# Optimization experiments

Hardware: AMD Instinct MI355X
Metric: run time of the kernel (lower is better)

## Reference

```python
import jax, jax.numpy as jnp
import numpy as np

N, E, G = 40000, 400000, 64
IN, ED, HID, HEADS, OUT = 2, 18, 64, 4, 3

def _glorot(key, shape):
    fan_in = shape[0]
    return jax.random.normal(key, shape, dtype=jnp.float32) / np.float32(np.sqrt(fan_in))

def setup_inputs():
    key = jax.random.key(0)
    ks = jax.random.split(key, 32)
    d1 = HEADS * HID  # 256
    return {
        "x": jax.random.normal(ks[0], (N, IN), jnp.float32),
        "edge_index": jax.random.randint(ks[1], (2, E), 0, N),
        "edge_attr": jax.random.normal(ks[2], (E, ED), jnp.float32),
        "batch": jnp.sort(jax.random.randint(ks[3], (N,), 0, G)),
        # conv1: TransformerConv(2 -> 64, heads=4, concat=True, beta=True, edge_dim=18)
        "Wq1": _glorot(ks[4], (IN, d1)), "bq1": jnp.zeros((d1,), jnp.float32),
        "Wk1": _glorot(ks[5], (IN, d1)), "bk1": jnp.zeros((d1,), jnp.float32),
        "Wv1": _glorot(ks[6], (IN, d1)), "bv1": jnp.zeros((d1,), jnp.float32),
        "We1": _glorot(ks[7], (ED, d1)),
        "Wskip1": _glorot(ks[8], (IN, d1)), "bskip1": jnp.zeros((d1,), jnp.float32),
        "Wbeta1": _glorot(ks[9], (3 * d1, 1)),
        # conv2: TransformerConv(256 -> 64, heads=1, concat=False, beta=True, edge_dim=18)
        "Wq2": _glorot(ks[10], (d1, HID)), "bq2": jnp.zeros((HID,), jnp.float32),
        "Wk2": _glorot(ks[11], (d1, HID)), "bk2": jnp.zeros((HID,), jnp.float32),
        "Wv2": _glorot(ks[12], (d1, HID)), "bv2": jnp.zeros((HID,), jnp.float32),
        "We2": _glorot(ks[13], (ED, HID)),
        "Wskip2": _glorot(ks[14], (d1, HID)), "bskip2": jnp.zeros((HID,), jnp.float32),
        "Wbeta2": _glorot(ks[15], (3 * HID, 1)),
        "Wlin": _glorot(ks[16], (HID, OUT)), "blin": jnp.zeros((OUT,), jnp.float32),
    }

def _tconv(x, src, dst, edge_attr, Wq, bq, Wk, bk, Wv, bv, We, Wskip, bskip, Wbeta, H, C, concat):
    # PyG TransformerConv with edge_dim, beta=True, root_weight=True (eval: dropout off)
    n = x.shape[0]
    q = (x @ Wq + bq).reshape(n, H, C)
    k = (x @ Wk + bk).reshape(n, H, C)
    v = (x @ Wv + bv).reshape(n, H, C)
    e = (edge_attr @ We).reshape(-1, H, C)              # [E,H,C]
    kj = k[src] + e                                      # key_j + edge
    alpha = jnp.einsum('ehc,ehc->eh', q[dst], kj) * (1.0 / (C ** 0.5))  # [E,H]
    # segment softmax over destination nodes
    amax = jax.ops.segment_max(alpha, dst, num_segments=n)
    ex = jnp.exp(alpha - amax[dst])
    den = jax.ops.segment_sum(ex, dst, num_segments=n)
    w = ex / (den[dst] + 1e-16)
    msg = (v[src] + e) * w[:, :, None]                   # [E,H,C]
    out = jax.ops.segment_sum(msg, dst, num_segments=n)  # [N,H,C]
    out = out.reshape(n, H * C) if concat else out.mean(axis=1)
    # beta-gated skip connection
    xr = x @ Wskip + bskip
    beta = jax.nn.sigmoid(jnp.concatenate([out, xr, out - xr], axis=-1) @ Wbeta)
    return beta * xr + (1.0 - beta) * out

def reference(x, edge_index, edge_attr, batch, Wq1, bq1, Wk1, bk1, Wv1, bv1, We1, Wskip1, bskip1, Wbeta1, Wq2, bq2, Wk2, bk2, Wv2, bv2, We2, Wskip2, bskip2, Wbeta2, Wlin, blin):
    src, dst = edge_index[0], edge_index[1]
    h = jax.nn.relu(_tconv(x, src, dst, edge_attr, Wq1, bq1, Wk1, bk1, Wv1, bv1, We1, Wskip1, bskip1, Wbeta1, HEADS, HID, True))
    h = jax.nn.relu(_tconv(h, src, dst, edge_attr, Wq2, bq2, Wk2, bk2, Wv2, bv2, We2, Wskip2, bskip2, Wbeta2, 1, HID, False))
    # global mean pool per graph
    s = jax.ops.segment_sum(h, batch, num_segments=G)
    cnt = jax.ops.segment_sum(jnp.ones((h.shape[0], 1), h.dtype), batch, num_segments=G)
    pooled = s / jnp.maximum(cnt, 1.0)
    return pooled @ Wlin + blin
```

## Files before the change

kernel.cpp:

```cpp
#include <hip/hip_runtime.h>
#include <hip/hip_fp16.h>

#define N_NODES 40000
#define N_EDGES 400000
#define N_GRAPHS 64
#define D1 256
#define HIDC 64
#define NHEADS 4
#define EDIM 18
#define EPAD 20
#define OUTF 3

typedef _Float16 f16x8 __attribute__((ext_vector_type(8)));
typedef float f32x4 __attribute__((ext_vector_type(4)));

__global__ void prep_w(const float* __restrict__ Wq, const float* __restrict__ bq,
                       const float* __restrict__ Wk, const float* __restrict__ bk,
                       const float* __restrict__ Wv, const float* __restrict__ bv,
                       const float* __restrict__ Ws, const float* __restrict__ bs,
                       const float* __restrict__ We2,
                       const float* __restrict__ Wq1, const float* __restrict__ bq1,
                       const float* __restrict__ Wk1, const float* __restrict__ bk1,
                       const float* __restrict__ We1,
                       __half* __restrict__ Bt, float* __restrict__ bias,
                       float* __restrict__ cbuf) {
    int c = blockIdx.x, k = threadIdx.x;
    if (c < 256) {
        int m = c >> 6, d = c & 63;
        const float* W = (m == 0) ? Wq : (m == 1) ? Wk : (m == 2) ? Wv : Ws;
        Bt[c * 256 + k] = __float2half(W[k * 64 + d]);
        if (k == 0) {
            const float* b = (m == 0) ? bq : (m == 1) ? bk : (m == 2) ? bv : bs;
            bias[c] = b[d];
        }
    } else if (c < 288) {
        int j = c - 256;
        float s = 0.f;
        if (j < EDIM)
            for (int cc = 0; cc < 64; ++cc) s += Wq[k * 64 + cc] * We2[j * 64 + cc];
        Bt[c * 256 + k] = __float2half(s);
        if (k == 0) {
            float b = 0.f;
            if (j < EDIM)
                for (int cc = 0; cc < 64; ++cc) b += bq[cc] * We2[j * 64 + cc];
            bias[c] = b;
        }
    } else {
        int t = k;
        if (t < 36) {
            int h = t / 9, r = t % 9, a = r / 3, b = r % 3;
            const float* A = (a == 0) ? Wq1 : (a == 1) ? Wq1 + D1 : bq1;
            const float* B = (b == 0) ? Wk1 : (b == 1) ? Wk1 + D1 : bk1;
            float s = 0.f;
            for (int cc = 0; cc < 64; ++cc) s += A[h * 64 + cc] * B[h * 64 + cc];
            cbuf[h * 63 + a * 3 + b] = s;
        } else if (t < 252) {
            int i = t - 36;
            int h = i / 54, rr = (i % 54) / 18, j = i % 18;
            const float* A = (rr == 0) ? Wq1 : (rr == 1) ? Wq1 + D1 : bq1;
            float s = 0.f;
            for (int cc = 0; cc < 64; ++cc) s += A[h * 64 + cc] * We1[j * D1 + h * 64 + cc];
            cbuf[h * 63 + 9 + rr * 18 + j] = s;
        }
    }
}

__global__ void initA(const float* __restrict__ x, const float* __restrict__ cbuf,
                      float* __restrict__ coef, float* __restrict__ acc1,
                      float* __restrict__ acc2, float* __restrict__ out2,
                      int* __restrict__ deg, float* __restrict__ pooled,
                      int* __restrict__ gs, int* __restrict__ ge) {
    int t = blockIdx.x * 256 + threadIdx.x;
    acc1[t] = 0.f;
    {
        int n = t / 84, r = t % 84, h = r / 21, c = r % 21;
        const float* cb = cbuf + h * 63;
        float x0 = x[2 * n], x1 = x[2 * n + 1], o;
        if (c < 3) o = x0 * cb[c] + x1 * cb[3 + c] + cb[6 + c];
        else { int j = c - 3; o = x0 * cb[9 + j] + x1 * cb[27 + j] + cb[45 + j]; }
        coef[t] = o;
    }
    if (t < N_NODES * 64) out2[t] = 0.f;
    if (t < N_NODES * 20) acc2[t] = 0.f;
    if (t < N_NODES) deg[t] = 0;
    if (t < N_GRAPHS * HIDC) pooled[t] = 0.f;
    if (t < N_GRAPHS) { gs[t] = 0; ge[t] = 0; }
}

__global__ void hist_kernel(const int* __restrict__ ei, int* __restrict__ deg) {
    int e = blockIdx.x * 256 + threadIdx.x;
    if (e < N_EDGES) atomicAdd(&deg[ei[N_EDGES + e]], 1);
}

__global__ void scanA(const int* __restrict__ deg, int* __restrict__ bsum) {
    __shared__ int s[256];
    int b = blockIdx.x, t = threadIdx.x;
    s[t] = (t < 160) ? deg[b * 160 + t] : 0;
    __syncthreads();
    for (int off = 128; off; off >>= 1) {
        if (t < off) s[t] += s[t + off];
        __syncthreads();
    }
    if (t == 0) bsum[b] = s[0];
}

__global__ void scanB(const int* __restrict__ bsum, int* __restrict__ boff) {
    __shared__ int s[256];
    int t = threadIdx.x;
    int v = (t < 250) ? bsum[t] : 0;
    s[t] = v;
    __syncthreads();
    for (int off = 1; off < 256; off <<= 1) {
        int add = (t >= off) ? s[t - off] : 0;
        __syncthreads();
        s[t] += add;
        __syncthreads();
    }
    if (t < 250) boff[t] = s[t] - v;
}

__global__ void scanC(const int* __restrict__ deg, const int* __restrict__ boff,
                      int* __restrict__ cursor) {
    __shared__ int s[256];
    int b = blockIdx.x, t = threadIdx.x;
    int v = (t < 160) ? deg[b * 160 + t] : 0;
    s[t] = v;
    __syncthreads();
    for (int off = 1; off < 256; off <<= 1) {
        int add = (t >= off) ? s[t - off] : 0;
        __syncthreads();
        s[t] += add;
        __syncthreads();
    }
    if (t < 160) cursor[b * 160 + t] = boff[b] + s[t] - v;
}

__global__ void perm_kernel(const int* __restrict__ ei, int* __restrict__ cursor,
                            int* __restrict__ inv) {
    int e = blockIdx.x * 256 + threadIdx.x;
    if (e >= N_EDGES) return;
    int p = atomicAdd(&cursor[ei[N_EDGES + e]], 1);
    inv[p] = e;
}

__global__ void gatherE(const int* __restrict__ inv, const int* __restrict__ ei,
                        const float* __restrict__ ea, const float* __restrict__ x,
                        const float* __restrict__ coef,
                        int* __restrict__ src_s, int* __restrict__ dst_s,
                        float* __restrict__ ea_s, float* __restrict__ alpha1) {
    int p = blockIdx.x * 256 + threadIdx.x;
    if (p >= N_EDGES) return;
    int e = inv[p];
    int src = ei[e], dst = ei[N_EDGES + e];
    src_s[p] = src;
    dst_s[p] = dst;
    const float* srow = ea + (size_t)e * EDIM;
    float s[EDIM];
    #pragma unroll
    for (int j = 0; j < EDIM; ++j) s[j] = srow[j];
    float x0 = x[src * 2], x1 = x[src * 2 + 1];
    float4* drow = (float4*)(ea_s + (size_t)p * EPAD);
    drow[0] = make_float4(s[0],  s[1],  s[2],  s[3]);
    drow[1] = make_float4(s[4],  s[5],  s[6],  s[7]);
    drow[2] = make_float4(s[8],  s[9],  s[10], s[11]);
    drow[3] = make_float4(s[12], s[13], s[14], s[15]);
    drow[4] = make_float4(s[16], s[17], x0, x1);
    const float* cb = coef + (size_t)dst * 84;
    #pragma unroll
    for (int h = 0; h < NHEADS; ++h) {
        const float* c = cb + h * 21;
        float a = x0 * c[0] + x1 * c[1] + c[2];
        #pragma unroll
        for (int j = 0; j < EDIM; ++j) a += s[j] * c[3 + j];
        alpha1[(size_t)h * N_EDGES + p] = __expf(a * 0.125f);
    }
}

__global__ void strip1(const int* __restrict__ dst_s, const float* __restrict__ alpha1,
                       const float* __restrict__ ea_s, float* __restrict__ acc1) {
    int t = threadIdx.x;
    int strip = blockIdx.x * 2 + (t >> 7);
    int gl = t & 127;
    bool active = gl < 84;
    int cgl = active ? gl : 83;
    int h = cgl / 21, comp = cgl % 21;
    int voff = (comp == 0) ? 18 : (comp == 1) ? 19 : (comp - 3);
    bool isone = (comp == 2);
    int p0 = strip * 16;
    int dsts[16]; float w[16]; float v[16];
    #pragma unroll
    for (int j = 0; j < 16; ++j) dsts[j] = dst_s[p0 + j];
    #pragma unroll
    for (int j = 0; j < 16; ++j) w[j] = alpha1[(size_t)h * N_EDGES + p0 + j];
    #pragma unroll
    for (int j = 0; j < 16; ++j) v[j] = isone ? 1.f : ea_s[(size_t)(p0 + j) * EPAD + voff];
    float acc = 0.f;
    int prev = dsts[0];
    #pragma unroll
    for (int j = 0; j < 16; ++j) {
        if (dsts[j] != prev) {
            if (active) atomicAdd(&acc1[(size_t)prev * 84 + gl], acc);
            acc = 0.f; prev = dsts[j];
        }
        acc += w[j] * v[j];
    }
    if (active) atomicAdd(&acc1[(size_t)prev * 84 + gl], acc);
}

__global__ void finalize1x(const float* __restrict__ x, const float* __restrict__ acc1,
                           const float* __restrict__ Wv, const float* __restrict__ bv,
                           const float* __restrict__ We, const float* __restrict__ Wskip,
                           const float* __restrict__ bskip, const float* __restrict__ Wbeta,
                           __half* __restrict__ h1f) {
    __shared__ float red[4][4];
    int nb = blockIdx.x * 4;
    int t = threadIdx.x;
    int h = t >> 6;
    float wv0 = Wv[t], wv1 = Wv[D1 + t], bvv = bv[t];
    float we[EDIM];
    #pragma unroll
    for (int j = 0; j < EDIM; ++j) we[j] = We[j * D1 + t];
    float ws0 = Wskip[t], ws1 = Wskip[D1 + t], bsv = bskip[t];
    float wb0 = Wbeta[t], wb1 = Wbeta[D1 + t], wb2 = Wbeta[2 * D1 + t];
    float o[4], xr[4], part[4];
    #pragma unroll
    for (int i = 0; i < 4; ++i) {
        int node = nb + i;
        const float* a = acc1 + (size_t)node * 84 + h * 21;
        float l = a[2];
        float oo = a[0] * wv0 + a[1] * wv1 + l * bvv;
        #pragma unroll
        for (int j = 0; j < EDIM; ++j) oo += a[3 + j] * we[j];
        oo /= (l + 1e-16f);
        float x0 = x[node * 2], x1 = x[node * 2 + 1];
        xr[i] = x0 * ws0 + x1 * ws1 + bsv;
        o[i] = oo;
        part[i] = oo * wb0 + xr[i] * wb1 + (oo - xr[i]) * wb2;
    }
    #pragma unroll
    for (int off = 32; off; off >>= 1) {
        #pragma unroll
        for (int i = 0; i < 4; ++i) part[i] += __shfl_xor(part[i], off);
    }
    if ((t & 63) == 0) {
        #pragma unroll
        for (int i = 0; i < 4; ++i) red[h][i] = part[i];
    }
    __syncthreads();
    #pragma unroll
    for (int i = 0; i < 4; ++i) {
        float tot = red[0][i] + red[1][i] + red[2][i] + red[3][i];
        float beta = 1.f / (1.f + __expf(-tot));
        h1f[(size_t)(nb + i) * D1 + t] =
            __float2half(fmaxf(beta * xr[i] + (1.f - beta) * o[i], 0.f));
    }
}

__device__ __forceinline__ void nl2_store(int c, int gr, float v,
        float* __restrict__ q2, float* __restrict__ k2, __half* __restrict__ v2h,
        float* __restrict__ xr2, float* __restrict__ qe) {
    if (c < 256) {
        int m = c >> 6, d = c & 63;
        if (m == 0)      q2[(size_t)gr * 64 + d] = v;
        else if (m == 1) k2[(size_t)gr * 64 + d] = v;
        else if (m == 2) v2h[(size_t)gr * 64 + d] = __float2half(v);
        else             xr2[(size_t)gr * 64 + d] = v;
    } else {
        qe[(size_t)gr * 32 + (c - 256)] = v;
    }
}

__global__ __launch_bounds__(256) void nl2_mfma(
        const __half* __restrict__ h1f, const __half* __restrict__ Bt,
        const float* __restrict__ bias,
        float* __restrict__ q2, float* __restrict__ k2,
        __half* __restrict__ v2h, float* __restrict__ xr2,
        float* __restrict__ qe) {
    int W = blockIdx.x * 4 + (threadIdx.x >> 6);
    if (W >= 18 * 313) return;
    int ct = W % 18, chunk = W / 18;
    int lane = threadIdx.x & 63, quad = lane >> 4, mm = lane & 15;
    int c0 = ct * 16 + mm;
    const _Float16* Ap = (const _Float16*)h1f;
    const _Float16* Bp = (const _Float16*)Bt;
    const _Float16* b0 = Bp + (size_t)c0 * 256 + quad * 8;
    f16x8 b[8];
    #pragma unroll
    for (int s = 0; s < 8; ++s) b[s] = *(const f16x8*)(b0 + s * 32);
    float bz = bias[c0];
    int rt_end = chunk * 8 + 8; if (rt_end > 2500) rt_end = 2500;
    for (int rt = chunk * 8; rt < rt_end; ++rt) {
        int row0 = rt * 16;
        const _Float16* arow = Ap + (size_t)(row0 + mm) * 256 + quad * 8;
        f16x8 a[8];
        #pragma unroll
        for (int s = 0; s < 8; ++s) a[s] = *(const f16x8*)(arow + s * 32);
        f32x4 accA = {bz, bz, bz, bz};
        f32x4 accB = {0.f, 0.f, 0.f, 0.f};
        #pragma unroll
        for (int s = 0; s < 4; ++s) {
            accA = __builtin_amdgcn_mfma_f32_16x16x32_f16(a[s],     b[s],     accA, 0, 0, 0);
            accB = __builtin_amdgcn_mfma_f32_16x16x32_f16(a[s + 4], b[s + 4], accB, 0, 0, 0);
        }
        #pragma unroll
        for (int r = 0; r < 4; ++r) {
            int gr = row0 + quad * 4 + r;
            nl2_store(c0, gr, accA[r] + accB[r], q2, k2, v2h, xr2, qe);
        }
    }
}

#define LG2_BLOCKS 2048
#define LG2_WAVES (LG2_BLOCKS * 4)
__global__ void logits2(const int* __restrict__ src_s, const int* __restrict__ dst_s,
                        const float* __restrict__ ea_s, const float* __restrict__ q2,
                        const float* __restrict__ k2, const float* __restrict__ qe,
                        float* __restrict__ alpha2) {
    int t = threadIdx.x, wid = t >> 6, lane = t & 63;
    int w = blockIdx.x * 4 + wid;
    for (int base = w; base < N_EDGES; base += 2 * LG2_WAVES) {
        int p1 = base, p2 = base + LG2_WAVES;
        bool has2 = p2 < N_EDGES;
        int p2c = has2 ? p2 : p1;
        int s1 = src_s[p1], d1 = dst_s[p1];
        int s2 = src_s[p2c], d2 = dst_s[p2c];
        float dd1 = q2[(size_t)d1 * 64 + lane] * k2[(size_t)s1 * 64 + lane];
        float dd2 = q2[(size_t)d2 * 64 + lane] * k2[(size_t)s2 * 64 + lane];
        if (lane < 20) {
            dd1 += qe[(size_t)d1 * 32 + lane] * ea_s[(size_t)p1 * EPAD + lane];
            dd2 += qe[(size_t)d2 * 32 + lane] * ea_s[(size_t)p2c * EPAD + lane];
        }
        #pragma unroll
        for (int off = 32; off; off >>= 1) {
            dd1 += __shfl_xor(dd1, off);
            dd2 += __shfl_xor(dd2, off);
        }
        if (lane == 0) {
            alpha2[p1] = __expf(dd1 * 0.125f);
            if (has2) alpha2[p2] = __expf(dd2 * 0.125f);
        }
    }
}

__global__ void spmm2s(const int* __restrict__ dst_s, const int* __restrict__ src_s,
                       const float* __restrict__ alpha2, const __half* __restrict__ v2h,
                       const float* __restrict__ ea_s,
                       float* __restrict__ out2, float* __restrict__ acc2) {
    int t = threadIdx.x;
    int strip = blockIdx.x * 4 + (t >> 6);
    int lane = t & 63;
    int p0 = strip * 16;
    int dsts[16]; int srcs[16]; float w[16];
    #pragma unroll
    for (int j = 0; j < 16; ++j) dsts[j] = dst_s[p0 + j];
    #pragma unroll
    for (int j = 0; j < 16; ++j) srcs[j] = src_s[p0 + j];
    #pragma unroll
    for (int j = 0; j < 16; ++j) w[j] = alpha2[p0 + j];
    float vv[16]; float ev[16];
    #pragma unroll
    for (int j = 0; j < 16; ++j) vv[j] = __half2float(v2h[(size_t)srcs[j] * 64 + lane]);
    #pragma unroll
    for (int j = 0; j < 16; ++j)
        ev[j] = (lane < EDIM) ? ea_s[(size_t)(p0 + j) * EPAD + lane] : 1.f;
    float acc = 0.f, accS = 0.f;
    int prev = dsts[0];
    #pragma unroll
    for (int j = 0; j < 16; ++j) {
        if (dsts[j] != prev) {
            atomicAdd(&out2[(size_t)prev * 64 + lane], acc);
            if (lane < 19) atomicAdd(&acc2[(size_t)prev * 20 + lane], accS);
            acc = 0.f; accS = 0.f; prev = dsts[j];
        }
        acc += w[j] * vv[j];
        accS += w[j] * ev[j];
    }
    atomicAdd(&out2[(size_t)prev * 64 + lane], acc);
    if (lane < 19) atomicAdd(&acc2[(size_t)prev * 20 + lane], accS);
}

__global__ void finalize2x(const float* __restrict__ out2, const float* __restrict__ acc2,
                           const float* __restrict__ xr2, const float* __restrict__ We2,
                           const float* __restrict__ Wb2, float* __restrict__ h2) {
    __shared__ float w2s[EDIM * 64];
    int t = threadIdx.x;
    for (int i = t; i < EDIM * 64; i += 256) w2s[i] = We2[i];
    __syncthreads();
    int node = blockIdx.x * 4 + (t >> 6);
    int lane = t & 63;
    const float* a2 = acc2 + (size_t)node * 20;
    float num = out2[(size_t)node * 64 + lane];
    #pragma unroll
    for (int j = 0; j < EDIM; ++j) num += a2[j] * w2s[j * 64 + lane];
    float o = num / (a2[18] + 1e-16f);
    float xr = xr2[(size_t)node * 64 + lane];
    float part = o * Wb2[lane] + xr * Wb2[64 + lane] + (o - xr) * Wb2[128 + lane];
    #pragma unroll
    for (int off = 32; off; off >>= 1) part += __shfl_xor(part, off);
    float beta = 1.f / (1.f + __expf(-part));
    h2[(size_t)node * 64 + lane] = fmaxf(beta * xr + (1.f - beta) * o, 0.f);
}

__global__ void bounds_kernel(const int* __restrict__ batch, int* __restrict__ gs,
                              int* __restrict__ ge) {
    int n = blockIdx.x * 256 + threadIdx.x;
    if (n >= N_NODES) return;
    int b = batch[n];
    if (n == 0) gs[b] = 0;
    else { int pb = batch[n - 1]; if (pb != b) { ge[pb] = n; gs[b] = n; } }
    if (n == N_NODES - 1) ge[b] = N_NODES;
}

__global__ void pool_kernel(const float* __restrict__ h2, const int* __restrict__ gs,
                            const int* __restrict__ ge, float* __restrict__ pooled,
                            float* __restrict__ cnt) {
    __shared__ float red[4][64];
    int g = blockIdx.x >> 2, q = blockIdx.x & 3;
    int t = threadIdx.x, wv = t >> 6, lane = t & 63;
    int s = gs[g], e = ge[g];
    float sum = 0.f;
    for (int n = s + q * 4 + wv; n < e; n += 16) sum += h2[(size_t)n * 64 + lane];
    red[wv][lane] = sum;
    __syncthreads();
    if (wv == 0) {
        float v = red[0][lane] + red[1][lane] + red[2][lane] + red[3][lane];
        atomicAdd(&pooled[g * 64 + lane], v);
    }
    if (q == 0 && t == 0) cnt[g] = (float)(e - s);
}

__global__ void final_lin(const float* __restrict__ pooled, const float* __restrict__ cnt,
                          const float* __restrict__ Wlin, const float* __restrict__ blin,
                          float* __restrict__ out) {
    int t = threadIdx.x;
    if (t >= N_GRAPHS * OUTF) return;
    int g = t / OUTF, o = t % OUTF;
    float inv = 1.f / fmaxf(cnt[g], 1.f);
    float acc = 0.f;
    for (int kk = 0; kk < HIDC; ++kk) acc += pooled[g * 64 + kk] * Wlin[kk * OUTF + o];
    out[t] = acc * inv + blin[o];
}

extern "C" void kernel_launch(void* const* d_in, const int* in_sizes, int n_in,
                              void* d_out, int out_size, void* d_ws, size_t ws_size,
                              hipStream_t stream) {
    const float* x      = (const float*)d_in[0];
    const int*   ei     = (const int*)d_in[1];
    const float* ea     = (const float*)d_in[2];
    const int*   batch  = (const int*)d_in[3];
    const float* Wq1    = (const float*)d_in[4];  const float* bq1    = (const float*)d_in[5];
    const float* Wk1    = (const float*)d_in[6];  const float* bk1    = (const float*)d_in[7];
    const float* Wv1    = (const float*)d_in[8];  const float* bv1    = (const float*)d_in[9];
    const float* We1    = (const float*)d_in[10];
    const float* Wskip1 = (const float*)d_in[11]; const float* bskip1 = (const float*)d_in[12];
    const float* Wbeta1 = (const float*)d_in[13];
    const float* Wq2    = (const float*)d_in[14]; const float* bq2    = (const float*)d_in[15];
    const float* Wk2    = (const float*)d_in[16]; const float* bk2    = (const float*)d_in[17];
    const float* Wv2    = (const float*)d_in[18]; const float* bv2    = (const float*)d_in[19];
    const float* We2    = (const float*)d_in[20];
    const float* Wskip2 = (const float*)d_in[21]; const float* bskip2 = (const float*)d_in[22];
    const float* Wbeta2 = (const float*)d_in[23];
    const float* Wlin   = (const float*)d_in[24]; const float* blin   = (const float*)d_in[25];

    float* ptr = (float*)d_ws;
    float* q2     = ptr; ptr += (size_t)N_NODES * 64;
    float* k2     = ptr; ptr += (size_t)N_NODES * 64;
    float* xr2    = ptr; ptr += (size_t)N_NODES * 64;
    float* qe     = ptr; ptr += (size_t)N_NODES * 32;
    __half* v2h   = (__half*)ptr; ptr += (size_t)N_NODES * 32;
    float* ea_s   = ptr; ptr += (size_t)N_EDGES * EPAD;
    float* alpha2 = ptr; ptr += N_EDGES;
    float* acc2   = ptr; ptr += (size_t)N_NODES * 20;
    float* out2   = ptr; ptr += (size_t)N_NODES * 64;
    float* pooled = ptr; ptr += N_GRAPHS * HIDC;
    float* cnt    = ptr; ptr += N_GRAPHS;
    int*   gs     = (int*)ptr; ptr += N_GRAPHS;
    int*   ge     = (int*)ptr; ptr += N_GRAPHS;
    float* cbuf   = ptr; ptr += 256;
    float* bias   = ptr; ptr += 320;
    __half* Bt    = (__half*)ptr; ptr += (288 * 256) / 2;
    int*   src_s  = (int*)ptr; ptr += N_EDGES;
    int*   dst_s  = (int*)ptr; ptr += N_EDGES;
    int*   inv    = (int*)ptr; ptr += N_EDGES;
    int*   deg    = (int*)ptr; ptr += N_NODES;
    int*   cursor = (int*)ptr; ptr += N_NODES;
    int*   bsum   = (int*)ptr; ptr += 256;
    int*   boff   = (int*)ptr; ptr += 256;
    float* coef   = ptr; ptr += (size_t)N_NODES * 84;
    float* h2     = coef;
    float* acc1   = ptr; ptr += (size_t)N_NODES * 84;
    float* alpha1 = ptr; ptr += (size_t)4 * N_EDGES;
    __half* h1f   = (__half*)ptr; ptr += (size_t)N_NODES * 128;

    const int EB = (N_EDGES + 255) / 256;
    const int NB = (N_NODES + 255) / 256;

    prep_w<<<289, 256, 0, stream>>>(Wq2, bq2, Wk2, bk2, Wv2, bv2, Wskip2, bskip2, We2,
                                    Wq1, bq1, Wk1, bk1, We1, Bt, bias, cbuf);
    initA<<<(N_NODES * 84) / 256, 256, 0, stream>>>(x, cbuf, coef, acc1, acc2, out2,
                                                    deg, pooled, gs, ge);
    hist_kernel<<<EB, 256, 0, stream>>>(ei, deg);
    scanA<<<250, 256, 0, stream>>>(deg, bsum);
    scanB<<<1, 256, 0, stream>>>(bsum, boff);
    scanC<<<250, 256, 0, stream>>>(deg, boff, cursor);
    perm_kernel<<<EB, 256, 0, stream>>>(ei, cursor, inv);
    gatherE<<<EB, 256, 0, stream>>>(inv, ei, ea, x, coef, src_s, dst_s, ea_s, alpha1);

    strip1<<<(N_EDGES / 16) / 2, 256, 0, stream>>>(dst_s, alpha1, ea_s, acc1);
    finalize1x<<<N_NODES / 4, 256, 0, stream>>>(x, acc1, Wv1, bv1, We1, Wskip1, bskip1,
                                                Wbeta1, h1f);

    nl2_mfma<<<1409, 256, 0, stream>>>(h1f, Bt, bias, q2, k2, v2h, xr2, qe);
    logits2<<<LG2_BLOCKS, 256, 0, stream>>>(src_s, dst_s, ea_s, q2, k2, qe, alpha2);
    spmm2s<<<(N_EDGES / 16) / 4, 256, 0, stream>>>(dst_s, src_s, alpha2, v2h, ea_s,
                                                   out2, acc2);
    finalize2x<<<N_NODES / 4, 256, 0, stream>>>(out2, acc2, xr2, We2, Wbeta2, h2);

    bounds_kernel<<<NB, 256, 0, stream>>>(batch, gs, ge);
    pool_kernel<<<N_GRAPHS * 4, 256, 0, stream>>>(h2, gs, ge, pooled, cnt);
    final_lin<<<1, 256, 0, stream>>>(pooled, cnt, Wlin, blin, (float*)d_out);
}
```

Measured before the change: 449.8 us.

## Fuse pooling into finalize2, merge scans, tile nl2 GEMM through LDS

After: 529.6 us. +17.8%, slower.

```diff
diff --git a/kernel.cpp b/kernel.cpp
--- a/kernel.cpp
+++ b/kernel.cpp
@@ -10,6 +10,7 @@
 #define EDIM 18
 #define EPAD 20
 #define OUTF 3
+#define APAD 264
 
 typedef _Float16 f16x8 __attribute__((ext_vector_type(8)));
 typedef float f32x4 __attribute__((ext_vector_type(4)));
@@ -87,52 +88,41 @@
     if (t < N_GRAPHS) { gs[t] = 0; ge[t] = 0; }
 }
 
-__global__ void hist_kernel(const int* __restrict__ ei, int* __restrict__ deg) {
+__global__ void hist_kernel(const int* __restrict__ ei, int* __restrict__ deg,
+                            const int* __restrict__ batch, int* __restrict__ gs,
+                            int* __restrict__ ge) {
     int e = blockIdx.x * 256 + threadIdx.x;
     if (e < N_EDGES) atomicAdd(&deg[ei[N_EDGES + e]], 1);
-}
-
-__global__ void scanA(const int* __restrict__ deg, int* __restrict__ bsum) {
-    __shared__ int s[256];
-    int b = blockIdx.x, t = threadIdx.x;
-    s[t] = (t < 160) ? deg[b * 160 + t] : 0;
+    int n = e;
+    if (n < N_NODES) {
+        int b = batch[n];
+        if (n == 0) gs[b] = 0;
+        else { int pb = batch[n - 1]; if (pb != b) { ge[pb] = n; gs[b] = n; } }
+        if (n == N_NODES - 1) ge[b] = N_NODES;
+    }
+}
+
+__global__ void scan_kernel(const int* __restrict__ deg, int* __restrict__ cursor) {
+    __shared__ int sums[1024];
+    int t = threadIdx.x;
+    const int PER = 40;
+    int base = t * PER;
+    int s = 0;
+    for (int i = 0; i < PER; ++i) { int idx = base + i; if (idx < N_NODES) s += deg[idx]; }
+    sums[t] = s;
     __syncthreads();
-    for (int off = 128; off; off >>= 1) {
-        if (t < off) s[t] += s[t + off];
+    for (int off = 1; off < 1024; off <<= 1) {
+        int v = sums[t];
+        int w = (t >= off) ? sums[t - off] : 0;
         __syncthreads();
-    }
-    if (t == 0) bsum[b] = s[0];
-}
-
-__global__ void scanB(const int* __restrict__ bsum, int* __restrict__ boff) {
-    __shared__ int s[256];
-    int t = threadIdx.x;
-    int v = (t < 250) ? bsum[t] : 0;
-    s[t] = v;
-    __syncthreads();
-    for (int off = 1; off < 256; off <<= 1) {
-        int add = (t >= off) ? s[t - off] : 0;
+        sums[t] = v + w;
         __syncthreads();
-        s[t] += add;
-        __syncthreads();
-    }
-    if (t < 250) boff[t] = s[t] - v;
-}
-
-__global__ void scanC(const int* __restrict__ deg, const int* __restrict__ boff,
-                      int* __restrict__ cursor) {
-    __shared__ int s[256];
-    int b = blockIdx.x, t = threadIdx.x;
-    int v = (t < 160) ? deg[b * 160 + t] : 0;
-    s[t] = v;
-    __syncthreads();
-    for (int off = 1; off < 256; off <<= 1) {
-        int add = (t >= off) ? s[t - off] : 0;
-        __syncthreads();
-        s[t] += add;
-        __syncthreads();
-    }
-    if (t < 160) cursor[b * 160 + t] = boff[b] + s[t] - v;
+    }
+    int run = (t == 0) ? 0 : sums[t - 1];
+    for (int i = 0; i < PER; ++i) {
+        int idx = base + i;
+        if (idx < N_NODES) { cursor[idx] = run; run += deg[idx]; }
+    }
 }
 
 __global__ void perm_kernel(const int* __restrict__ ei, int* __restrict__ cursor,
@@ -276,36 +266,44 @@
         float* __restrict__ q2, float* __restrict__ k2,
         __half* __restrict__ v2h, float* __restrict__ xr2,
         float* __restrict__ qe) {
-    int W = blockIdx.x * 4 + (threadIdx.x >> 6);
-    if (W >= 18 * 313) return;
-    int ct = W % 18, chunk = W / 18;
-    int lane = threadIdx.x & 63, quad = lane >> 4, mm = lane & 15;
-    int c0 = ct * 16 + mm;
-    const _Float16* Ap = (const _Float16*)h1f;
+    __shared__ _Float16 As[64 * APAD];
+    int t = threadIdx.x;
+    int row0 = blockIdx.x * 64;
+    const float4* gsrc = (const float4*)(h1f + (size_t)row0 * 256);
+    #pragma unroll
+    for (int i = 0; i < 8; ++i) {
+        int li = i * 256 + t;
+        int r = li >> 5, c8 = li & 31;
+        *(float4*)(As + r * APAD + c8 * 8) = gsrc[li];
+    }
+    __syncthreads();
+    int wave = t >> 6, lane = t & 63, quad = lane >> 4, mm = lane & 15;
     const _Float16* Bp = (const _Float16*)Bt;
-    const _Float16* b0 = Bp + (size_t)c0 * 256 + quad * 8;
-    f16x8 b[8];
-    #pragma unroll
-    for (int s = 0; s < 8; ++s) b[s] = *(const f16x8*)(b0 + s * 32);
-    float bz = bias[c0];
-    int rt_end = chunk * 8 + 8; if (rt_end > 2500) rt_end = 2500;
-    for (int rt = chunk * 8; rt < rt_end; ++rt) {
-        int row0 = rt * 16;
-        const _Float16* arow = Ap + (size_t)(row0 + mm) * 256 + quad * 8;
-        f16x8 a[8];
-        #pragma unroll
-        for (int s = 0; s < 8; ++s) a[s] = *(const f16x8*)(arow + s * 32);
-        f32x4 accA = {bz, bz, bz, bz};
-        f32x4 accB = {0.f, 0.f, 0.f, 0.f};
-        #pragma unroll
-        for (int s = 0; s < 4; ++s) {
-            accA = __builtin_amdgcn_mfma_f32_16x16x32_f16(a[s],     b[s],     accA, 0, 0, 0);
-            accB = __builtin_amdgcn_mfma_f32_16x16x32_f16(a[s + 4], b[s + 4], accB, 0, 0, 0);
-        }
-        #pragma unroll
-        for (int r = 0; r < 4; ++r) {
-            int gr = row0 + quad * 4 + r;
-            nl2_store(c0, gr, accA[r] + accB[r], q2, k2, v2h, xr2, qe);
+    for (int ct = wave; ct < 18; ct += 4) {
+        int c0 = ct * 16 + mm;
+        const _Float16* b0 = Bp + (size_t)c0 * 256 + quad * 8;
+        f16x8 b[8];
+        #pragma unroll
+        for (int s = 0; s < 8; ++s) b[s] = *(const f16x8*)(b0 + s * 32);
+        float bz = bias[c0];
+        #pragma unroll
+        for (int rt = 0; rt < 4; ++rt) {
+            const _Float16* arow = As + (rt * 16 + mm) * APAD + quad * 8;
+            f16x8 a[8];
+            #pragma unroll
+            for (int s = 0; s < 8; ++s) a[s] = *(const f16x8*)(arow + s * 32);
+            f32x4 accA = {bz, bz, bz, bz};
+            f32x4 accB = {0.f, 0.f, 0.f, 0.f};
+            #pragma unroll
+            for (int s = 0; s < 4; ++s) {
+                accA = __builtin_amdgcn_mfma_f32_16x16x32_f16(a[s],     b[s],     accA, 0, 0, 0);
+                accB = __builtin_amdgcn_mfma_f32_16x16x32_f16(a[s + 4], b[s + 4], accB, 0, 0, 0);
+            }
+            #pragma unroll
+            for (int r = 0; r < 4; ++r) {
+                int gr = row0 + rt * 16 + quad * 4 + r;
+                nl2_store(c0, gr, accA[r] + accB[r], q2, k2, v2h, xr2, qe);
+            }
         }
     }
 }
@@ -381,7 +379,8 @@
 
 __global__ void finalize2x(const float* __restrict__ out2, const float* __restrict__ acc2,
                            const float* __restrict__ xr2, const float* __restrict__ We2,
-                           const float* __restrict__ Wb2, float* __restrict__ h2) {
+                           const float* __restrict__ Wb2, const int* __restrict__ batch,
+                           float* __restrict__ pooled) {
     __shared__ float w2s[EDIM * 64];
     int t = threadIdx.x;
     for (int i = t; i < EDIM * 64; i += 256) w2s[i] = We2[i];
@@ -398,44 +397,19 @@
     #pragma unroll
     for (int off = 32; off; off >>= 1) part += __shfl_xor(part, off);
     float beta = 1.f / (1.f + __expf(-part));
-    h2[(size_t)node * 64 + lane] = fmaxf(beta * xr + (1.f - beta) * o, 0.f);
-}
-
-__global__ void bounds_kernel(const int* __restrict__ batch, int* __restrict__ gs,
-                              int* __restrict__ ge) {
-    int n = blockIdx.x * 256 + threadIdx.x;
-    if (n >= N_NODES) return;
-    int b = batch[n];
-    if (n == 0) gs[b] = 0;
-    else { int pb = batch[n - 1]; if (pb != b) { ge[pb] = n; gs[b] = n; } }
-    if (n == N_NODES - 1) ge[b] = N_NODES;
-}
-
-__global__ void pool_kernel(const float* __restrict__ h2, const int* __restrict__ gs,
-                            const int* __restrict__ ge, float* __restrict__ pooled,
-                            float* __restrict__ cnt) {
-    __shared__ float red[4][64];
-    int g = blockIdx.x >> 2, q = blockIdx.x & 3;
-    int t = threadIdx.x, wv = t >> 6, lane = t & 63;
-    int s = gs[g], e = ge[g];
-    float sum = 0.f;
-    for (int n = s + q * 4 + wv; n < e; n += 16) sum += h2[(size_t)n * 64 + lane];
-    red[wv][lane] = sum;
-    __syncthreads();
-    if (wv == 0) {
-        float v = red[0][lane] + red[1][lane] + red[2][lane] + red[3][lane];
-        atomicAdd(&pooled[g * 64 + lane], v);
-    }
-    if (q == 0 && t == 0) cnt[g] = (float)(e - s);
-}
-
-__global__ void final_lin(const float* __restrict__ pooled, const float* __restrict__ cnt,
+    float hh = fmaxf(beta * xr + (1.f - beta) * o, 0.f);
+    atomicAdd(&pooled[batch[node] * 64 + lane], hh);
+}
+
+__global__ void final_lin(const float* __restrict__ pooled, const int* __restrict__ gs,
+                          const int* __restrict__ ge,
                           const float* __restrict__ Wlin, const float* __restrict__ blin,
                           float* __restrict__ out) {
     int t = threadIdx.x;
     if (t >= N_GRAPHS * OUTF) return;
     int g = t / OUTF, o = t % OUTF;
-    float inv = 1.f / fmaxf(cnt[g], 1.f);
+    int c = ge[g] - gs[g];
+    float inv = 1.f / fmaxf((float)c, 1.f);
     float acc = 0.f;
     for (int kk = 0; kk < HIDC; ++kk) acc += pooled[g * 64 + kk] * Wlin[kk * OUTF + o];
     out[t] = acc * inv + blin[o];
@@ -473,7 +447,6 @@
     float* acc2   = ptr; ptr += (size_t)N_NODES * 20;
     float* out2   = ptr; ptr += (size_t)N_NODES * 64;
     float* pooled = ptr; ptr += N_GRAPHS * HIDC;
-    float* cnt    = ptr; ptr += N_GRAPHS;
     int*   gs     = (int*)ptr; ptr += N_GRAPHS;
     int*   ge     = (int*)ptr; ptr += N_GRAPHS;
     float* cbuf   = ptr; ptr += 256;
@@ -484,25 +457,19 @@
     int*   inv    = (int*)ptr; ptr += N_EDGES;
     int*   deg    = (int*)ptr; ptr += N_NODES;
     int*   cursor = (int*)ptr; ptr += N_NODES;
-    int*   bsum   = (int*)ptr; ptr += 256;
-    int*   boff   = (int*)ptr; ptr += 256;
     float* coef   = ptr; ptr += (size_t)N_NODES * 84;
-    float* h2     = coef;
     float* acc1   = ptr; ptr += (size_t)N_NODES * 84;
     float* alpha1 = ptr; ptr += (size_t)4 * N_EDGES;
     __half* h1f   = (__half*)ptr; ptr += (size_t)N_NODES * 128;
 
     const int EB = (N_EDGES + 255) / 256;
-    const int NB = (N_NODES + 255) / 256;
 
     prep_w<<<289, 256, 0, stream>>>(Wq2, bq2, Wk2, bk2, Wv2, bv2, Wskip2, bskip2, We2,
                                     Wq1, bq1, Wk1, bk1, We1, Bt, bias, cbuf);
     initA<<<(N_NODES * 84) / 256, 256, 0, stream>>>(x, cbuf, coef, acc1, acc2, out2,
                                                     deg, pooled, gs, ge);
-    hist_kernel<<<EB, 256, 0, stream>>>(ei, deg);
-    scanA<<<250, 256, 0, stream>>>(deg, bsum);
-    scanB<<<1, 256, 0, stream>>>(bsum, boff);
-    scanC<<<250, 256, 0, stream>>>(deg, boff, cursor);
+    hist_kernel<<<EB, 256, 0, stream>>>(ei, deg, batch, gs, ge);
+    scan_kernel<<<1, 1024, 0, stream>>>(deg, cursor);
     perm_kernel<<<EB, 256, 0, stream>>>(ei, cursor, inv);
     gatherE<<<EB, 256, 0, stream>>>(inv, ei, ea, x, coef, src_s, dst_s, ea_s, alpha1);
 
@@ -510,13 +477,11 @@
     finalize1x<<<N_NODES / 4, 256, 0, stream>>>(x, acc1, Wv1, bv1, We1, Wskip1, bskip1,
                                                 Wbeta1, h1f);
 
-    nl2_mfma<<<1409, 256, 0, stream>>>(h1f, Bt, bias, q2, k2, v2h, xr2, qe);
+    nl2_mfma<<<N_NODES / 64, 256, 0, stream>>>(h1f, Bt, bias, q2, k2, v2h, xr2, qe);
     logits2<<<LG2_BLOCKS, 256, 0, stream>>>(src_s, dst_s, ea_s, q2, k2, qe, alpha2);
     spmm2s<<<(N_EDGES / 16) / 4, 256, 0, stream>>>(dst_s, src_s, alpha2, v2h, ea_s,
                                                    out2, acc2);
-    finalize2x<<<N_NODES / 4, 256, 0, stream>>>(out2, acc2, xr2, We2, Wbeta2, h2);
-
-    bounds_kernel<<<NB, 256, 0, stream>>>(batch, gs, ge);
-    pool_kernel<<<N_GRAPHS * 4, 256, 0, stream>>>(h2, gs, ge, pooled, cnt);
-    final_lin<<<1, 256, 0, stream>>>(pooled, cnt, Wlin, blin, (float*)d_out);
-}
+    finalize2x<<<N_NODES / 4, 256, 0, stream>>>(out2, acc2, xr2, We2, Wbeta2, batch, pooled);
+
+    final_lin<<<1, 256, 0, stream>>>(pooled, gs, ge, Wlin, blin, (float*)d_out);
+}
```
